# Optimization experiments

Measured on AMD Instinct MI355X. Metric: run time of the kernel, lower is better.

Reference implementation:

```python
import jax, jax.numpy as jnp
import numpy as np

B, K, NUM_CLASS = 16, 256, 18
# strictly-upper-triangle pairs in row-major order, matching torch.nonzero(tril-masked dist < 3)
_iu = np.triu_indices(K, 1)
PAIRS = jnp.stack([jnp.asarray(_iu[0], jnp.int32), jnp.asarray(_iu[1], jnp.int32)], axis=1)  # (P,2)


def _box_intervals(center, size, heading):
    # vectorized getXyz: vectors = diag(diag(size) * R(heading)) = size * [h1, 1, h1]
    h1 = heading[:, 1:2]
    vectors = size * jnp.concatenate([h1, jnp.ones_like(h1), h1], axis=-1)
    low = vectors + center - jnp.abs(size)
    high = vectors + center
    # per-proposal axis-aligned interval [lx,hx,ly,hy,lz,hz]
    return jnp.stack([low[:, 0], high[:, 0], low[:, 1], high[:, 1], low[:, 2], high[:, 2]], axis=-1)  # (K,6)


def _suppress(center, size, heading, scores):
    # center/size (K,3), heading (K,2), scores (K,2); sequential pairwise suppression
    d = _box_intervals(center, size, heading)

    def step(scores, pij):
        i, j = pij[0], pij[1]
        active = jnp.sum((center[i] - center[j]) ** 2) < 9.0  # ||ci-cj|| < 3
        d1, d2 = d[i], d[j]
        case0 = (d2[0] < d1[0]) & (d2[1] > d1[1]) & (d2[2] < d1[2]) & (d2[3] > d1[3]) & (d2[4] < d1[4]) & (d2[5] > d1[5])
        case1 = (d2[0] > d1[0]) & (d2[1] < d1[1]) & (d2[2] > d1[2]) & (d2[3] < d1[3]) & (d2[4] > d1[4]) & (d2[5] < d1[5])

        def ov(lo1, hi1, lo2, hi2):
            return ((hi2 > lo1) & (hi2 < hi1)) | ((hi1 > lo2) & (hi1 < hi2))

        case2 = ov(d1[0], d1[1], d2[0], d2[1]) & ov(d1[2], d1[3], d2[2], d2[3]) & ov(d1[4], d1[5], d2[4], d2[5])
        zp, zn = scores[i, 0], scores[i, 1]
        fp, fn = scores[j, 0], scores[j, 1]
        c2 = (~case0) & (~case1) & case2
        swap_i = active & ((case0 & (zp < zn)) | (c2 & (zn < fn)))
        swap_j = active & ((((~case0) & case1) & (fp < fn)) | (c2 & ~(zn < fn)))
        scores = scores.at[i].set(jnp.where(swap_i, jnp.stack([zn, zp]), jnp.stack([zp, zn])))
        scores = scores.at[j].set(jnp.where(swap_j, jnp.stack([fn, fp]), jnp.stack([fp, fn])))
        return scores, None

    scores, _ = jax.lax.scan(step, scores, PAIRS)
    return scores


def _forward(pred_center, pred_size, pred_heading, sem_obj_feature, aggregated_vote_xyz):
    # decode_scores
    center = aggregated_vote_xyz + jnp.transpose(pred_center, (0, 2, 1))  # (B,K,3)
    size = jnp.transpose(pred_size, (0, 2, 1))                           # (B,K,3)
    heading = jnp.transpose(pred_heading, (0, 2, 1))                     # (B,K,2)
    sem_obj = jnp.transpose(sem_obj_feature, (0, 2, 1))                  # (B,K,2+NUM_CLASS)
    obj = jax.vmap(_suppress)(center, size, heading, sem_obj[..., 0:2])  # post_process
    sem_cls = sem_obj[..., 2:]
    return jnp.concatenate([center, size, heading, obj, sem_cls], axis=-1)  # (B,K,28)


def setup_inputs() -> dict:
    key = jax.random.key(0)
    k1, k2, k3, k4, k5 = jax.random.split(key, 5)
    return {
        "pred_center": jax.random.normal(k1, (B, 3, K), jnp.float32) * 0.2,
        "pred_size": jax.random.uniform(k2, (B, 3, K), jnp.float32, minval=0.1, maxval=2.0),
        "pred_heading": jax.random.normal(k3, (B, 2, K), jnp.float32),
        "sem_obj_feature": jax.random.normal(k4, (B, 2 + NUM_CLASS, K), jnp.float32),
        "aggregated_vote_xyz": jax.random.normal(k5, (B, K, 3), jnp.float32) * 3.0,
    }


def reference(pred_center, pred_size, pred_heading, sem_obj_feature, aggregated_vote_xyz):
    return _forward(pred_center, pred_size, pred_heading, sem_obj_feature, aggregated_vote_xyz)
```

## Files before the change

kernel.cpp:

```cpp
#include <hip/hip_runtime.h>

#define KK 256
#define NCLS 18
#define MASK_BYTES_PER_BATCH (KK * KK)

typedef unsigned long long ull;

__global__ __launch_bounds__(256)
void flags_kernel(const float* __restrict__ pc, const float* __restrict__ ps,
                  const float* __restrict__ ph, const float* __restrict__ sem,
                  const float* __restrict__ av,
                  unsigned char* __restrict__ ws_mask,
                  unsigned char* __restrict__ ws_sum,
                  float* __restrict__ out)
{
#pragma clang fp contract(off)
    const int blk = blockIdx.x;
    const int b   = blk >> 4;
    const int g   = blk & 15;
    const int tid = threadIdx.x;

    __shared__ float sd0[KK], sd1[KK], sd2[KK], sd3[KK], sd4[KK], sd5[KK];
    __shared__ float sp[KK], sn[KK], sc0[KK], sc1[KK], sc2[KK];
    __shared__ unsigned rowsum[16];

    const float* pcb  = pc  + (size_t)b * 3 * KK;
    const float* psb  = ps  + (size_t)b * 3 * KK;
    const float* phb  = ph  + (size_t)b * 2 * KK;
    const float* semb = sem + (size_t)b * (2 + NCLS) * KK;
    const float* avb  = av  + (size_t)b * KK * 3;
    float* outb       = out + (size_t)b * KK * 28;

    {
        const int k = tid;
        const float c0 = avb[k*3+0] + pcb[0*KK + k];
        const float c1 = avb[k*3+1] + pcb[1*KK + k];
        const float c2 = avb[k*3+2] + pcb[2*KK + k];
        const float s0 = psb[0*KK + k], s1 = psb[1*KK + k], s2 = psb[2*KK + k];
        const float h1 = phb[1*KK + k];
        const float v0 = s0 * h1, v1 = s1, v2 = s2 * h1;
        sd0[k] = (v0 + c0) - fabsf(s0);
        sd1[k] = (v0 + c0);
        sd2[k] = (v1 + c1) - fabsf(s1);
        sd3[k] = (v1 + c1);
        sd4[k] = (v2 + c2) - fabsf(s2);
        sd5[k] = (v2 + c2);
        sp[k]  = semb[0*KK + k];
        sn[k]  = semb[1*KK + k];
        sc0[k] = c0; sc1[k] = c1; sc2[k] = c2;
    }
    if (tid < 16) rowsum[tid] = 0;
    __syncthreads();

    const int rl = tid & 15;
    const int i  = g * 16 + rl;
    const int j0 = (tid >> 4) * 16;

    const float piv = sp[i], niv = sn[i];
    const float di0 = sd0[i], di1 = sd1[i], di2 = sd2[i];
    const float di3 = sd3[i], di4 = sd4[i], di5 = sd5[i];
    const float ci0 = sc0[i], ci1 = sc1[i], ci2 = sc2[i];

    unsigned W[4] = {0u, 0u, 0u, 0u};
    bool evt = false;
#pragma unroll
    for (int t = 0; t < 16; ++t) {
        const int j = j0 + t;
        unsigned a0 = 1u, a1 = 1u, b0 = 0u, b1 = 0u, isC = 0u, mm0 = 0u, mm1 = 1u;
        if (j > i) {
            const float dx = ci0 - sc0[j];
            const float dy = ci1 - sc1[j];
            const float dz = ci2 - sc2[j];
            const float dist2 = dx*dx + dy*dy + dz*dz;
            if (dist2 < 9.0f) {
                const float e0 = sd0[j], e1 = sd1[j], e2 = sd2[j];
                const float e3 = sd3[j], e4 = sd4[j], e5 = sd5[j];
                const bool case0 = (e0 < di0) & (e1 > di1) & (e2 < di2)
                                 & (e3 > di3) & (e4 < di4) & (e5 > di5);
                const bool case1 = (e0 > di0) & (e1 < di1) & (e2 > di2)
                                 & (e3 < di3) & (e4 > di4) & (e5 < di5);
                if (case0) {
                    const unsigned tA0 = (piv < niv) ? 1u : 0u;
                    const unsigned tA1 = (niv < piv) ? 0u : 1u;
                    a0 = a1 = tA0 ^ tA1;
                    b0 = b1 = tA0;
                    evt = true;
                } else if (case1) {
                    const float pjv = sp[j], njv = sn[j];
                    mm0 = (pjv < njv) ? 1u : 0u;
                    mm1 = (njv < pjv) ? 0u : 1u;
                    evt = true;
                } else {
                    const bool ovx = ((e1 > di0) & (e1 < di1)) | ((di1 > e0) & (di1 < e1));
                    const bool ovy = ((e3 > di2) & (e3 < di3)) | ((di3 > e2) & (di3 < e3));
                    const bool ovz = ((e5 > di4) & (e5 < di5)) | ((di5 > e4) & (di5 < e5));
                    if (ovx & ovy & ovz) {
                        const float pjv = sp[j], njv = sn[j];
                        const unsigned c00 = (niv < njv) ? 1u : 0u;
                        const unsigned c10 = (piv < njv) ? 1u : 0u;
                        const unsigned c01 = (niv < pjv) ? 1u : 0u;
                        const unsigned c11 = (piv < pjv) ? 1u : 0u;
                        isC = 1u;
                        a0 = 1u ^ c00 ^ c10;  b0 = c00;
                        a1 = 1u ^ c01 ^ c11;  b1 = c01;
                        evt = true;
                    }
                }
            }
        }
        const unsigned s = a0 | (a1 << 4) | (b0 << 8) | (b1 << 12)
                         | (isC << 16) | (mm0 << 20) | (mm1 << 24);
        W[t >> 2] |= s << (t & 3);
    }

    uint4 w4;
    w4.x = W[0]; w4.y = W[1]; w4.z = W[2]; w4.w = W[3];
    *(uint4*)(ws_mask + (size_t)b * MASK_BYTES_PER_BATCH + i * KK + j0) = w4;

    if (evt) atomicOr(&rowsum[rl], 1u);

    for (int s = tid; s < 16 * 28; s += 256) {
        const int kk = g * 16 + (s / 28);
        const int c  = s % 28;
        if (c == 8 || c == 9) continue;
        float val;
        if (c < 3)       val = (c == 0) ? sc0[kk] : ((c == 1) ? sc1[kk] : sc2[kk]);
        else if (c < 6)  val = psb[(c - 3) * KK + kk];
        else if (c < 8)  val = phb[(c - 6) * KK + kk];
        else             val = semb[(c - 8) * KK + kk];
        outb[(size_t)kk * 28 + c] = val;
    }

    __syncthreads();
    if (tid < 16) {
        ws_sum[b * KK + g * 16 + tid] = (unsigned char)rowsum[tid];
    }
}

__global__ __launch_bounds__(64)
void suppress7_kernel(const float* __restrict__ sem,
                      const unsigned char* __restrict__ ws_mask,
                      const unsigned char* __restrict__ ws_sum,
                      float* __restrict__ out)
{
    const int b    = blockIdx.x;
    const int lane = threadIdx.x;

    __shared__ unsigned s_mask[KK * 64];

    const float* semb = sem + (size_t)b * (2 + NCLS) * KK;
    float* outb       = out + (size_t)b * KK * 28;

    const uint4* gm = (const uint4*)(ws_mask + (size_t)b * MASK_BYTES_PER_BATCH);
    uint4* sm4 = (uint4*)s_mask;
    for (int so = 0; so < 64; so += 8) {
        uint4 v[8];
#pragma unroll
        for (int t = 0; t < 8; ++t) v[t] = gm[(so + t) * 64 + lane];
#pragma unroll
        for (int t = 0; t < 8; ++t) sm4[(so + t) * 64 + lane] = v[t];
    }

    float pj[4], nj[4];
#pragma unroll
    for (int q = 0; q < 4; ++q) {
        const int k = lane * 4 + q;
        pj[q] = semb[0*KK + k];
        nj[q] = semb[1*KK + k];
    }

    const unsigned char* sbp = ws_sum + b * KK;
    const unsigned sb0 = sbp[lane], sb1 = sbp[64 + lane],
                   sb2 = sbp[128 + lane], sb3 = sbp[192 + lane];
    const ull any0 = __ballot(sb0 & 1u);
    const ull any1 = __ballot(sb1 & 1u);
    const ull any2 = __ballot(sb2 & 1u);
    const ull any3 = __ballot(sb3 & 1u);

    __syncthreads();

    unsigned bmask = 0;
    const ull belowR = __builtin_bitreverse64((1ull << lane) - 1ull);

#define ROWBODY(i_) { \
        const unsigned m = mcur; \
        const int slot = (i_) & 3, owner = (i_) >> 2; \
        const ull bsb = __ballot(((bmask >> slot) & 1u) != 0u); \
        const unsigned b_start = (unsigned)((bsb >> owner) & 1ull); \
        const unsigned A0n = m & 0xFu,         A1n = (m >> 4) & 0xFu; \
        const unsigned B0n = (m >> 8) & 0xFu,  B1n = (m >> 12) & 0xFu; \
        const unsigned isCn = (m >> 16) & 0xFu; \
        const unsigned M0n = (m >> 20) & 0xFu, M1n = (m >> 24) & 0xFu; \
        const unsigned bm = bmask; \
        const unsigned AV  = (A1n & bm) | (A0n & ~bm); \
        const unsigned BV  = (B1n & bm) | (B0n & ~bm); \
        const unsigned bmB = (M1n & bm) | (M0n & ~bm); \
        const unsigned F0s = isCn & ~BV; \
        const unsigned F1s = isCn & (AV ^ BV); \
         \
        const unsigned As = AV << 1; \
        const unsigned Bs = BV << 1; \
        const unsigned B2 = Bs ^ (As & (Bs << 1)); \
        const unsigned A2 = As & (As << 1); \
        const unsigned av0 = B2 ^ (A2 & (B2 << 2)); \
        const unsigned y  = As | 1u; \
        const unsigned z1 = y & ((y << 1) | 1u); \
        const unsigned pa = z1 & ((z1 << 2) | 3u); \
        const unsigned FS  = (AV & av0) ^ BV;    \
        const unsigned aTv = pa & AV;            \
        const ull b0m = __ballot((FS & 8u) != 0u); \
        const ull b1m = __ballot(((FS ^ aTv) & 8u) != 0u); \
         \
        const ull nm  = b0m & ~b1m; \
        const ull cm  = ~(b0m ^ b1m); \
        const ull cmr = __builtin_bitreverse64(cm); \
        const ull nmr = __builtin_bitreverse64(nm); \
        const ull Wr  = __builtin_bitreverse64(b0m); \
        const ull cbr = cmr & belowR; \
        const ull lb  = cbr & (0ull - cbr); \
        const unsigned vK = ((Wr & lb) != 0ull) ? 1u : 0u; \
        const ull betw = belowR & (lb - 1ull); \
        const unsigned par = (unsigned)__builtin_popcountll(nmr & betw) & 1u; \
        const unsigned excl = ((cbr != 0ull) ? vK : b_start) ^ par; \
        const ull lbA = cmr & (0ull - cmr); \
        const unsigned vKA = ((Wr & lbA) != 0ull) ? 1u : 0u; \
        const unsigned parA = (unsigned)__builtin_popcountll(nmr & (lbA - 1ull)) & 1u; \
        const unsigned bfin = ((cmr != 0ull) ? vKA : b_start) ^ parA; \
         \
        const unsigned Emask = (0u - excl) & 0xFu; \
        const unsigned sv = av0 ^ (pa & Emask); \
        const unsigned flips = (F1s & sv) | (F0s & ~sv); \
        unsigned nbm = bmB ^ flips; \
        const unsigned fixed = (nbm & ~(1u << slot)) | (bfin << slot); \
        bmask = (lane == owner) ? fixed : nbm; }

#define RUNCHUNK(W_, ANY, NROWS) \
    for (int bb = 0; bb < (NROWS); ++bb) { \
        const int i_ = ((W_) << 6) + bb; \
        const unsigned mnext = s_mask[(i_ + 1) * 64 + lane]; \
        if (((ANY) >> bb) & 1ull) ROWBODY(i_) \
        mcur = mnext; \
    }

    unsigned mcur = s_mask[lane];
    RUNCHUNK(0, any0, 64)
    RUNCHUNK(1, any1, 64)
    RUNCHUNK(2, any2, 64)
    RUNCHUNK(3, any3, 63)

#undef RUNCHUNK
#undef ROWBODY

#pragma unroll
    for (int q = 0; q < 4; ++q) {
        const int k = lane * 4 + q;
        const unsigned bq = (bmask >> q) & 1u;
        outb[k*28 + 8] = bq ? nj[q] : pj[q];
        outb[k*28 + 9] = bq ? pj[q] : nj[q];
    }
}

__device__ __forceinline__ unsigned compose2(unsigned a, unsigned b) {
    unsigned r0 = (b >> (a & 1u)) & 1u;
    unsigned r1 = (b >> ((a >> 1) & 1u)) & 1u;
    return r0 | (r1 << 1u);
}

__global__ __launch_bounds__(64)
void proposal_suppress_kernel(const float* __restrict__ pc, const float* __restrict__ ps,
                              const float* __restrict__ ph, const float* __restrict__ sem,
                              const float* __restrict__ av, float* __restrict__ out)
{
#pragma clang fp contract(off)
    const int b    = blockIdx.x;
    const int lane = threadIdx.x;

    __shared__ float s_p[KK], s_n[KK], s_d[KK][6], s_c[KK][3];

    const float* pcb  = pc  + (size_t)b * 3 * KK;
    const float* psb  = ps  + (size_t)b * 3 * KK;
    const float* phb  = ph  + (size_t)b * 2 * KK;
    const float* semb = sem + (size_t)b * (2 + NCLS) * KK;
    const float* avb  = av  + (size_t)b * KK * 3;
    float* outb       = out + (size_t)b * KK * 28;

    float pj[4], nj[4], dj[4][6], cj[4][3];
    unsigned Ljm = 0, Gjm = 0, bmask = 0;

#pragma unroll
    for (int q = 0; q < 4; ++q) {
        const int k = lane * 4 + q;
        const float c0 = avb[k*3+0] + pcb[0*KK + k];
        const float c1 = avb[k*3+1] + pcb[1*KK + k];
        const float c2 = avb[k*3+2] + pcb[2*KK + k];
        const float s0 = psb[0*KK + k], s1 = psb[1*KK + k], s2 = psb[2*KK + k];
        const float h0 = phb[0*KK + k], h1 = phb[1*KK + k];
        const float v0 = s0 * h1, v1 = s1, v2 = s2 * h1;
        float d[6];
        d[0] = (v0 + c0) - fabsf(s0); d[1] = (v0 + c0);
        d[2] = (v1 + c1) - fabsf(s1); d[3] = (v1 + c1);
        d[4] = (v2 + c2) - fabsf(s2); d[5] = (v2 + c2);
        const float p = semb[0*KK + k];
        const float n = semb[1*KK + k];
        cj[q][0] = c0; cj[q][1] = c1; cj[q][2] = c2;
#pragma unroll
        for (int m = 0; m < 6; ++m) dj[q][m] = d[m];
        pj[q] = p; nj[q] = n;
        if (p < n) Ljm |= 1u << q;
        if (n < p) Gjm |= 1u << q;
        s_p[k] = p; s_n[k] = n;
#pragma unroll
        for (int m = 0; m < 6; ++m) s_d[k][m] = d[m];
        s_c[k][0] = c0; s_c[k][1] = c1; s_c[k][2] = c2;
        outb[k*28 + 0] = c0; outb[k*28 + 1] = c1; outb[k*28 + 2] = c2;
        outb[k*28 + 3] = s0; outb[k*28 + 4] = s1; outb[k*28 + 5] = s2;
        outb[k*28 + 6] = h0; outb[k*28 + 7] = h1;
#pragma unroll
        for (int cc = 0; cc < NCLS; ++cc)
            outb[k*28 + 10 + cc] = semb[(2 + cc)*KK + k];
    }
    __syncthreads();

    const unsigned ID = 2u;
    for (int i = 0; i < KK - 1; ++i) {
        const float piv = s_p[i], niv = s_n[i];
        const float di0 = s_d[i][0], di1 = s_d[i][1], di2 = s_d[i][2];
        const float di3 = s_d[i][3], di4 = s_d[i][4], di5 = s_d[i][5];
        const float ci0 = s_c[i][0], ci1 = s_c[i][1], ci2 = s_c[i][2];
        const unsigned tA = (piv < niv ? 1u : 0u) | ((niv < piv ? 0u : 1u) << 1);
        const int owner = i >> 2, slot = i & 3;

        unsigned tq[4];
        unsigned Cq = 0, cc0m = 0, cc1m = 0;
        unsigned tl = ID;
#pragma unroll
        for (int q = 0; q < 4; ++q) {
            const int j = lane * 4 + q;
            unsigned t = ID;
            if (j > i) {
                const float dx = ci0 - cj[q][0];
                const float dy = ci1 - cj[q][1];
                const float dz = ci2 - cj[q][2];
                const float dist2 = dx*dx + dy*dy + dz*dz;
                if (dist2 < 9.0f) {
                    const bool case0 = (dj[q][0] < di0) & (dj[q][1] > di1)
                                     & (dj[q][2] < di2) & (dj[q][3] > di3)
                                     & (dj[q][4] < di4) & (dj[q][5] > di5);
                    const bool case1 = (dj[q][0] > di0) & (dj[q][1] < di1)
                                     & (dj[q][2] > di2) & (dj[q][3] < di3)
                                     & (dj[q][4] > di4) & (dj[q][5] < di5);
                    if (case0) {
                        t = tA;
                    } else if (case1) {
                        const unsigned bj = (bmask >> q) & 1u;
                        const unsigned nb = bj ? (((Gjm >> q) & 1u) ? 0u : 1u)
                                               : (((Ljm >> q) & 1u) ? 1u : 0u);
                        bmask = (bmask & ~(1u << q)) | (nb << q);
                    } else {
                        const bool ovx = ((dj[q][1] > di0) & (dj[q][1] < di1))
                                       | ((di1 > dj[q][0]) & (di1 < dj[q][1]));
                        const bool ovy = ((dj[q][3] > di2) & (dj[q][3] < di3))
                                       | ((di3 > dj[q][2]) & (di3 < dj[q][3]));
                        const bool ovz = ((dj[q][5] > di4) & (dj[q][5] < di5))
                                       | ((di5 > dj[q][4]) & (di5 < dj[q][5]));
                        if (ovx & ovy & ovz) {
                            const unsigned bj = (bmask >> q) & 1u;
                            const float sj = bj ? pj[q] : nj[q];
                            const unsigned c0b = (niv < sj) ? 1u : 0u;
                            const unsigned c1b = (piv < sj) ? 1u : 0u;
                            t = c0b | ((c1b ^ 1u) << 1u);
                            Cq |= 1u << q; cc0m |= c0b << q; cc1m |= c1b << q;
                        }
                    }
                }
            }
            tq[q] = t;
            tl = compose2(tl, t);
        }

        const ull any = __ballot((tl != ID) || (Cq != 0));
        if (any == 0ull) continue;

        const unsigned b_start = (((unsigned)__shfl((int)bmask, owner, 64)) >> slot) & 1u;

        unsigned incl = tl;
#pragma unroll
        for (int off = 1; off < 64; off <<= 1) {
            const unsigned other = (unsigned)__shfl_up((int)incl, (unsigned)off, 64);
            if (lane >= off) incl = compose2(other, incl);
        }
        const unsigned total = (unsigned)__shfl((int)incl, 63, 64);
        const unsigned upv   = (unsigned)__shfl_up((int)incl, 1u, 64);
        const unsigned excl  = (lane == 0) ? ID : upv;

        unsigned cur = (excl >> b_start) & 1u;
#pragma unroll
        for (int q = 0; q < 4; ++q) {
            if ((Cq >> q) & 1u) {
                const unsigned cond = cur ? ((cc1m >> q) & 1u) : ((cc0m >> q) & 1u);
                if (!cond) bmask ^= (1u << q);
            }
            cur = (tq[q] >> cur) & 1u;
        }
        if (lane == owner) {
            const unsigned nbi = (total >> b_start) & 1u;
            bmask = (bmask & ~(1u << slot)) | (nbi << slot);
        }
    }

#pragma unroll
    for (int q = 0; q < 4; ++q) {
        const int k = lane * 4 + q;
        const unsigned bq = (bmask >> q) & 1u;
        outb[k*28 + 8] = bq ? nj[q] : pj[q];
        outb[k*28 + 9] = bq ? pj[q] : nj[q];
    }
}

extern "C" void kernel_launch(void* const* d_in, const int* in_sizes, int n_in,
                              void* d_out, int out_size, void* d_ws, size_t ws_size,
                              hipStream_t stream) {
    const float* pc  = (const float*)d_in[0];
    const float* ps  = (const float*)d_in[1];
    const float* ph  = (const float*)d_in[2];
    const float* sem = (const float*)d_in[3];
    const float* av  = (const float*)d_in[4];
    float* out = (float*)d_out;
    const int B = in_sizes[0] / (3 * KK);

    const size_t need = (size_t)B * MASK_BYTES_PER_BATCH + (size_t)B * KK;
    if (ws_size >= need) {
        unsigned char* wm   = (unsigned char*)d_ws;
        unsigned char* wsum = wm + (size_t)B * MASK_BYTES_PER_BATCH;
        flags_kernel<<<dim3(B * 16), dim3(256), 0, stream>>>(pc, ps, ph, sem, av, wm, wsum, out);
        suppress7_kernel<<<dim3(B), dim3(64), 0, stream>>>(sem, wm, wsum, out);
    } else {
        proposal_suppress_kernel<<<dim3(B), dim3(64), 0, stream>>>(pc, ps, ph, sem, av, out);
    }
}
```

Measured before the change: 43.98 us.

## Replace row-skip flags with branchless log-step parallel prefix scan in suppression

Removes the per-row event summary (rowsum atomics, extra sync and ws_sum buffer) from the flags kernel, so the suppression kernel no longer skips rows with no interactions. The cross-lane carry in each row changes from bit-reverse, lowest-set-bit and popcount logic to a six-step log-shift scan over the 64-bit ballot masks. Both outcomes for each lane are computed and one is picked per lane. This shortens the serial dependency chain per row and drops a workspace write and a barrier, but every one of the 255 rows is now processed even when it has no events.

Result: slower. 78.69 us (+78.9%).

```diff
diff --git a/kernel.cpp b/kernel.cpp
--- a/kernel.cpp
+++ b/kernel.cpp
@@ -11,7 +11,6 @@
                   const float* __restrict__ ph, const float* __restrict__ sem,
                   const float* __restrict__ av,
                   unsigned char* __restrict__ ws_mask,
-                  unsigned char* __restrict__ ws_sum,
                   float* __restrict__ out)
 {
 #pragma clang fp contract(off)
@@ -22,7 +21,6 @@
 
     __shared__ float sd0[KK], sd1[KK], sd2[KK], sd3[KK], sd4[KK], sd5[KK];
     __shared__ float sp[KK], sn[KK], sc0[KK], sc1[KK], sc2[KK];
-    __shared__ unsigned rowsum[16];
 
     const float* pcb  = pc  + (size_t)b * 3 * KK;
     const float* psb  = ps  + (size_t)b * 3 * KK;
@@ -49,7 +47,6 @@
         sn[k]  = semb[1*KK + k];
         sc0[k] = c0; sc1[k] = c1; sc2[k] = c2;
     }
-    if (tid < 16) rowsum[tid] = 0;
     __syncthreads();
 
     const int rl = tid & 15;
@@ -62,7 +59,6 @@
     const float ci0 = sc0[i], ci1 = sc1[i], ci2 = sc2[i];
 
     unsigned W[4] = {0u, 0u, 0u, 0u};
-    bool evt = false;
 #pragma unroll
     for (int t = 0; t < 16; ++t) {
         const int j = j0 + t;
@@ -84,12 +80,10 @@
                     const unsigned tA1 = (niv < piv) ? 0u : 1u;
                     a0 = a1 = tA0 ^ tA1;
                     b0 = b1 = tA0;
-                    evt = true;
                 } else if (case1) {
                     const float pjv = sp[j], njv = sn[j];
                     mm0 = (pjv < njv) ? 1u : 0u;
                     mm1 = (njv < pjv) ? 0u : 1u;
-                    evt = true;
                 } else {
                     const bool ovx = ((e1 > di0) & (e1 < di1)) | ((di1 > e0) & (di1 < e1));
                     const bool ovy = ((e3 > di2) & (e3 < di3)) | ((di3 > e2) & (di3 < e3));
@@ -103,7 +97,6 @@
                         isC = 1u;
                         a0 = 1u ^ c00 ^ c10;  b0 = c00;
                         a1 = 1u ^ c01 ^ c11;  b1 = c01;
-                        evt = true;
                     }
                 }
             }
@@ -116,8 +109,6 @@
     uint4 w4;
     w4.x = W[0]; w4.y = W[1]; w4.z = W[2]; w4.w = W[3];
     *(uint4*)(ws_mask + (size_t)b * MASK_BYTES_PER_BATCH + i * KK + j0) = w4;
-
-    if (evt) atomicOr(&rowsum[rl], 1u);
 
     for (int s = tid; s < 16 * 28; s += 256) {
         const int kk = g * 16 + (s / 28);
@@ -130,17 +121,11 @@
         else             val = semb[(c - 8) * KK + kk];
         outb[(size_t)kk * 28 + c] = val;
     }
-
-    __syncthreads();
-    if (tid < 16) {
-        ws_sum[b * KK + g * 16 + tid] = (unsigned char)rowsum[tid];
-    }
 }
 
 __global__ __launch_bounds__(64)
-void suppress7_kernel(const float* __restrict__ sem,
+void suppress8_kernel(const float* __restrict__ sem,
                       const unsigned char* __restrict__ ws_mask,
-                      const unsigned char* __restrict__ ws_sum,
                       float* __restrict__ out)
 {
     const int b    = blockIdx.x;
@@ -169,87 +154,72 @@
         nj[q] = semb[1*KK + k];
     }
 
-    const unsigned char* sbp = ws_sum + b * KK;
-    const unsigned sb0 = sbp[lane], sb1 = sbp[64 + lane],
-                   sb2 = sbp[128 + lane], sb3 = sbp[192 + lane];
-    const ull any0 = __ballot(sb0 & 1u);
-    const ull any1 = __ballot(sb1 & 1u);
-    const ull any2 = __ballot(sb2 & 1u);
-    const ull any3 = __ballot(sb3 & 1u);
-
     __syncthreads();
 
     unsigned bmask = 0;
-    const ull belowR = __builtin_bitreverse64((1ull << lane) - 1ull);
-
-#define ROWBODY(i_) { \
-        const unsigned m = mcur; \
-        const int slot = (i_) & 3, owner = (i_) >> 2; \
-        const ull bsb = __ballot(((bmask >> slot) & 1u) != 0u); \
-        const unsigned b_start = (unsigned)((bsb >> owner) & 1ull); \
-        const unsigned A0n = m & 0xFu,         A1n = (m >> 4) & 0xFu; \
-        const unsigned B0n = (m >> 8) & 0xFu,  B1n = (m >> 12) & 0xFu; \
-        const unsigned isCn = (m >> 16) & 0xFu; \
-        const unsigned M0n = (m >> 20) & 0xFu, M1n = (m >> 24) & 0xFu; \
-        const unsigned bm = bmask; \
-        const unsigned AV  = (A1n & bm) | (A0n & ~bm); \
-        const unsigned BV  = (B1n & bm) | (B0n & ~bm); \
-        const unsigned bmB = (M1n & bm) | (M0n & ~bm); \
-        const unsigned F0s = isCn & ~BV; \
-        const unsigned F1s = isCn & (AV ^ BV); \
-         \
-        const unsigned As = AV << 1; \
-        const unsigned Bs = BV << 1; \
-        const unsigned B2 = Bs ^ (As & (Bs << 1)); \
-        const unsigned A2 = As & (As << 1); \
-        const unsigned av0 = B2 ^ (A2 & (B2 << 2)); \
-        const unsigned y  = As | 1u; \
-        const unsigned z1 = y & ((y << 1) | 1u); \
-        const unsigned pa = z1 & ((z1 << 2) | 3u); \
-        const unsigned FS  = (AV & av0) ^ BV;    \
-        const unsigned aTv = pa & AV;            \
-        const ull b0m = __ballot((FS & 8u) != 0u); \
-        const ull b1m = __ballot(((FS ^ aTv) & 8u) != 0u); \
-         \
-        const ull nm  = b0m & ~b1m; \
-        const ull cm  = ~(b0m ^ b1m); \
-        const ull cmr = __builtin_bitreverse64(cm); \
-        const ull nmr = __builtin_bitreverse64(nm); \
-        const ull Wr  = __builtin_bitreverse64(b0m); \
-        const ull cbr = cmr & belowR; \
-        const ull lb  = cbr & (0ull - cbr); \
-        const unsigned vK = ((Wr & lb) != 0ull) ? 1u : 0u; \
-        const ull betw = belowR & (lb - 1ull); \
-        const unsigned par = (unsigned)__builtin_popcountll(nmr & betw) & 1u; \
-        const unsigned excl = ((cbr != 0ull) ? vK : b_start) ^ par; \
-        const ull lbA = cmr & (0ull - cmr); \
-        const unsigned vKA = ((Wr & lbA) != 0ull) ? 1u : 0u; \
-        const unsigned parA = (unsigned)__builtin_popcountll(nmr & (lbA - 1ull)) & 1u; \
-        const unsigned bfin = ((cmr != 0ull) ? vKA : b_start) ^ parA; \
-         \
-        const unsigned Emask = (0u - excl) & 0xFu; \
-        const unsigned sv = av0 ^ (pa & Emask); \
-        const unsigned flips = (F1s & sv) | (F0s & ~sv); \
-        unsigned nbm = bmB ^ flips; \
-        const unsigned fixed = (nbm & ~(1u << slot)) | (bfin << slot); \
-        bmask = (lane == owner) ? fixed : nbm; }
-
-#define RUNCHUNK(W_, ANY, NROWS) \
-    for (int bb = 0; bb < (NROWS); ++bb) { \
-        const int i_ = ((W_) << 6) + bb; \
-        const unsigned mnext = s_mask[(i_ + 1) * 64 + lane]; \
-        if (((ANY) >> bb) & 1ull) ROWBODY(i_) \
-        mcur = mnext; \
-    }
-
     unsigned mcur = s_mask[lane];
-    RUNCHUNK(0, any0, 64)
-    RUNCHUNK(1, any1, 64)
-    RUNCHUNK(2, any2, 64)
-    RUNCHUNK(3, any3, 63)
-
-#undef RUNCHUNK
-#undef ROWBODY
+
+    for (int i = 0; i < KK - 1; ++i) {
+        const unsigned mnext = s_mask[(i + 1) * 64 + lane];
+        const unsigned m = mcur;
+        const int slot = i & 3, owner = i >> 2;
+
+        const ull bsb = __ballot(((bmask >> slot) & 1u) != 0u);
+
+        const unsigned A0n = m & 0xFu,         A1n = (m >> 4) & 0xFu;
+        const unsigned B0n = (m >> 8) & 0xFu,  B1n = (m >> 12) & 0xFu;
+        const unsigned isCn = (m >> 16) & 0xFu;
+        const unsigned M0n = (m >> 20) & 0xFu, M1n = (m >> 24) & 0xFu;
+        const unsigned bm = bmask;
+        const unsigned AV  = (A1n & bm) | (A0n & ~bm);
+        const unsigned BV  = (B1n & bm) | (B0n & ~bm);
+        const unsigned bmB = (M1n & bm) | (M0n & ~bm);
+        const unsigned F0s = isCn & ~BV;
+        const unsigned F1s = isCn & (AV ^ BV);
+
+        const unsigned As = AV << 1;
+        const unsigned Bs = BV << 1;
+        const unsigned B2 = Bs ^ (As & (Bs << 1));
+        const unsigned A2 = As & (As << 1);
+        const unsigned av0 = B2 ^ (A2 & (B2 << 2));
+        const unsigned y  = As | 1u;
+        const unsigned z1 = y & ((y << 1) | 1u);
+        const unsigned pa = z1 & ((z1 << 2) | 3u);
+        const unsigned FS  = (AV & av0) ^ BV;
+        const unsigned aTv = pa & AV;
+
+        const ull b0m = __ballot((FS & 8u) != 0u);
+        const ull b1m = __ballot(((FS ^ aTv) & 8u) != 0u);
+
+        const unsigned sv1 = av0 ^ pa;
+        const unsigned flips0 = (F1s & av0) | (F0s & ~av0);
+        const unsigned flips1 = (F1s & sv1) | (F0s & ~sv1);
+        const unsigned nbm0 = bmB ^ flips0;
+        const unsigned nbm1 = bmB ^ flips1;
+
+        const ull amask = b0m ^ b1m;
+        ull A = (amask << 1) | 1ull;
+        ull B = b0m << 1;
+        B ^= A & (B << 1);  A &= (A << 1)  | 1ull;
+        B ^= A & (B << 2);  A &= (A << 2)  | 3ull;
+        B ^= A & (B << 4);  A &= (A << 4)  | 15ull;
+        B ^= A & (B << 8);  A &= (A << 8)  | 255ull;
+        B ^= A & (B << 16); A &= (A << 16) | 0xFFFFull;
+        B ^= A & (B << 32); A &= (A << 32) | 0xFFFFFFFFull;
+        const unsigned b_start = (unsigned)((bsb >> owner) & 1ull);
+        const ull EW = B ^ (b_start ? A : 0ull);
+        const unsigned bfin = (unsigned)(((amask & EW) ^ b0m) >> 63) & 1u;
+
+        const unsigned keep = ~(1u << slot);
+        const unsigned ins  = bfin << slot;
+        const unsigned fixed0 = (lane == owner) ? ((nbm0 & keep) | ins) : nbm0;
+        const unsigned fixed1 = (lane == owner) ? ((nbm1 & keep) | ins) : nbm1;
+
+        const unsigned El = (unsigned)((EW >> lane) & 1ull);
+        bmask = El ? fixed1 : fixed0;
+
+        mcur = mnext;
+    }
 
 #pragma unroll
     for (int q = 0; q < 4; ++q) {
@@ -428,12 +398,11 @@
     float* out = (float*)d_out;
     const int B = in_sizes[0] / (3 * KK);
 
-    const size_t need = (size_t)B * MASK_BYTES_PER_BATCH + (size_t)B * KK;
+    const size_t need = (size_t)B * MASK_BYTES_PER_BATCH;
     if (ws_size >= need) {
-        unsigned char* wm   = (unsigned char*)d_ws;
-        unsigned char* wsum = wm + (size_t)B * MASK_BYTES_PER_BATCH;
-        flags_kernel<<<dim3(B * 16), dim3(256), 0, stream>>>(pc, ps, ph, sem, av, wm, wsum, out);
-        suppress7_kernel<<<dim3(B), dim3(64), 0, stream>>>(sem, wm, wsum, out);
+        unsigned char* wm = (unsigned char*)d_ws;
+        flags_kernel<<<dim3(B * 16), dim3(256), 0, stream>>>(pc, ps, ph, sem, av, wm, out);
+        suppress8_kernel<<<dim3(B), dim3(64), 0, stream>>>(sem, wm, out);
     } else {
         proposal_suppress_kernel<<<dim3(B), dim3(64), 0, stream>>>(pc, ps, ph, sem, av, out);
     }
```

## Process two batches per wavefront in suppression kernel to interleave serial chains

Applied to the files above, without the earlier changes.

The sequential suppression kernel now handles two batch elements per 64-lane block, interleaving their per-row dependency chains so the latency of ballots and bit operations in one chain can be hidden by the other. The grid is halved and LDS use doubles to 128KB per block. The cost is fewer blocks (8 instead of 16) and longer per-block work. The gain depends on whether interleaving two serial chains hides latency better than running them on separate CUs.

Result: slower. 64.25 us (+46.1%).

```diff
diff --git a/kernel.cpp b/kernel.cpp
--- a/kernel.cpp
+++ b/kernel.cpp
@@ -138,60 +138,78 @@
 }
 
 __global__ __launch_bounds__(64)
-void suppress7_kernel(const float* __restrict__ sem,
-                      const unsigned char* __restrict__ ws_mask,
-                      const unsigned char* __restrict__ ws_sum,
-                      float* __restrict__ out)
+void suppress11_kernel(const float* __restrict__ sem,
+                       const unsigned char* __restrict__ ws_mask,
+                       const unsigned char* __restrict__ ws_sum,
+                       float* __restrict__ out, int B)
 {
-    const int b    = blockIdx.x;
+    const int pb   = blockIdx.x;
+    const int bA   = pb * 2;
+    const int bBr  = pb * 2 + 1;
+    const bool hasB = (bBr < B);
+    const int bB   = hasB ? bBr : bA;
     const int lane = threadIdx.x;
 
-    __shared__ unsigned s_mask[KK * 64];
-
-    const float* semb = sem + (size_t)b * (2 + NCLS) * KK;
-    float* outb       = out + (size_t)b * KK * 28;
-
-    const uint4* gm = (const uint4*)(ws_mask + (size_t)b * MASK_BYTES_PER_BATCH);
-    uint4* sm4 = (uint4*)s_mask;
+    __shared__ unsigned s_mask[2 * KK * 64];
+
+    const float* sembA = sem + (size_t)bA * (2 + NCLS) * KK;
+    const float* sembB = sem + (size_t)bB * (2 + NCLS) * KK;
+    float* outbA = out + (size_t)bA * KK * 28;
+    float* outbB = out + (size_t)bB * KK * 28;
+
+    const uint4* gmA = (const uint4*)(ws_mask + (size_t)bA * MASK_BYTES_PER_BATCH);
+    const uint4* gmB = (const uint4*)(ws_mask + (size_t)bB * MASK_BYTES_PER_BATCH);
+    uint4* smA = (uint4*)s_mask;
+    uint4* smB = (uint4*)(s_mask + KK * 64);
     for (int so = 0; so < 64; so += 8) {
-        uint4 v[8];
-#pragma unroll
-        for (int t = 0; t < 8; ++t) v[t] = gm[(so + t) * 64 + lane];
-#pragma unroll
-        for (int t = 0; t < 8; ++t) sm4[(so + t) * 64 + lane] = v[t];
-    }
-
-    float pj[4], nj[4];
+        uint4 v[8], w[8];
+#pragma unroll
+        for (int t = 0; t < 8; ++t) v[t] = gmA[(so + t) * 64 + lane];
+#pragma unroll
+        for (int t = 0; t < 8; ++t) w[t] = gmB[(so + t) * 64 + lane];
+#pragma unroll
+        for (int t = 0; t < 8; ++t) smA[(so + t) * 64 + lane] = v[t];
+#pragma unroll
+        for (int t = 0; t < 8; ++t) smB[(so + t) * 64 + lane] = w[t];
+    }
+
+    float pjA[4], njA[4], pjB[4], njB[4];
 #pragma unroll
     for (int q = 0; q < 4; ++q) {
         const int k = lane * 4 + q;
-        pj[q] = semb[0*KK + k];
-        nj[q] = semb[1*KK + k];
-    }
-
-    const unsigned char* sbp = ws_sum + b * KK;
-    const unsigned sb0 = sbp[lane], sb1 = sbp[64 + lane],
-                   sb2 = sbp[128 + lane], sb3 = sbp[192 + lane];
-    const ull any0 = __ballot(sb0 & 1u);
-    const ull any1 = __ballot(sb1 & 1u);
-    const ull any2 = __ballot(sb2 & 1u);
-    const ull any3 = __ballot(sb3 & 1u);
+        pjA[q] = sembA[0*KK + k];
+        njA[q] = sembA[1*KK + k];
+        pjB[q] = sembB[0*KK + k];
+        njB[q] = sembB[1*KK + k];
+    }
+
+    const unsigned char* sbA = ws_sum + bA * KK;
+    const unsigned char* sbB = ws_sum + bB * KK;
+    const unsigned a0 = sbA[lane], a1 = sbA[64 + lane],
+                   a2 = sbA[128 + lane], a3 = sbA[192 + lane];
+    const unsigned e0 = sbB[lane], e1 = sbB[64 + lane],
+                   e2 = sbB[128 + lane], e3 = sbB[192 + lane];
+    const ull anyA0 = __ballot(a0 & 1u), anyA1 = __ballot(a1 & 1u),
+              anyA2 = __ballot(a2 & 1u), anyA3 = __ballot(a3 & 1u);
+    ull anyB0 = __ballot(e0 & 1u), anyB1 = __ballot(e1 & 1u),
+        anyB2 = __ballot(e2 & 1u), anyB3 = __ballot(e3 & 1u);
+    if (!hasB) { anyB0 = anyB1 = anyB2 = anyB3 = 0ull; }
 
     __syncthreads();
 
-    unsigned bmask = 0;
+    unsigned bmaskA = 0, bmaskB = 0;
     const ull belowR = __builtin_bitreverse64((1ull << lane) - 1ull);
 
-#define ROWBODY(i_) { \
-        const unsigned m = mcur; \
+#define ROWBODY(i_, MW, BMV) { \
+        const unsigned m = (MW); \
         const int slot = (i_) & 3, owner = (i_) >> 2; \
-        const ull bsb = __ballot(((bmask >> slot) & 1u) != 0u); \
+        const ull bsb = __ballot(((BMV >> slot) & 1u) != 0u); \
         const unsigned b_start = (unsigned)((bsb >> owner) & 1ull); \
         const unsigned A0n = m & 0xFu,         A1n = (m >> 4) & 0xFu; \
         const unsigned B0n = (m >> 8) & 0xFu,  B1n = (m >> 12) & 0xFu; \
         const unsigned isCn = (m >> 16) & 0xFu; \
         const unsigned M0n = (m >> 20) & 0xFu, M1n = (m >> 24) & 0xFu; \
-        const unsigned bm = bmask; \
+        const unsigned bm = BMV; \
         const unsigned AV  = (A1n & bm) | (A0n & ~bm); \
         const unsigned BV  = (B1n & bm) | (B0n & ~bm); \
         const unsigned bmB = (M1n & bm) | (M0n & ~bm); \
@@ -232,21 +250,24 @@
         const unsigned flips = (F1s & sv) | (F0s & ~sv); \
         unsigned nbm = bmB ^ flips; \
         const unsigned fixed = (nbm & ~(1u << slot)) | (bfin << slot); \
-        bmask = (lane == owner) ? fixed : nbm; }
-
-#define RUNCHUNK(W_, ANY, NROWS) \
+        BMV = (lane == owner) ? fixed : nbm; }
+
+#define RUNCHUNK(W_, ANYA, ANYB, NROWS) \
     for (int bb = 0; bb < (NROWS); ++bb) { \
         const int i_ = ((W_) << 6) + bb; \
-        const unsigned mnext = s_mask[(i_ + 1) * 64 + lane]; \
-        if (((ANY) >> bb) & 1ull) ROWBODY(i_) \
-        mcur = mnext; \
-    }
-
-    unsigned mcur = s_mask[lane];
-    RUNCHUNK(0, any0, 64)
-    RUNCHUNK(1, any1, 64)
-    RUNCHUNK(2, any2, 64)
-    RUNCHUNK(3, any3, 63)
+        const unsigned mnextA = s_mask[(i_ + 1) * 64 + lane]; \
+        const unsigned mnextB = s_mask[KK * 64 + (i_ + 1) * 64 + lane]; \
+        if (((ANYA) >> bb) & 1ull) ROWBODY(i_, mcurA, bmaskA) \
+        if (((ANYB) >> bb) & 1ull) ROWBODY(i_, mcurB, bmaskB) \
+        mcurA = mnextA; mcurB = mnextB; \
+    }
+
+    unsigned mcurA = s_mask[lane];
+    unsigned mcurB = s_mask[KK * 64 + lane];
+    RUNCHUNK(0, anyA0, anyB0, 64)
+    RUNCHUNK(1, anyA1, anyB1, 64)
+    RUNCHUNK(2, anyA2, anyB2, 64)
+    RUNCHUNK(3, anyA3, anyB3, 63)
 
 #undef RUNCHUNK
 #undef ROWBODY
@@ -254,9 +275,18 @@
 #pragma unroll
     for (int q = 0; q < 4; ++q) {
         const int k = lane * 4 + q;
-        const unsigned bq = (bmask >> q) & 1u;
-        outb[k*28 + 8] = bq ? nj[q] : pj[q];
-        outb[k*28 + 9] = bq ? pj[q] : nj[q];
+        const unsigned bqA = (bmaskA >> q) & 1u;
+        outbA[k*28 + 8] = bqA ? njA[q] : pjA[q];
+        outbA[k*28 + 9] = bqA ? pjA[q] : njA[q];
+    }
+    if (hasB) {
+#pragma unroll
+        for (int q = 0; q < 4; ++q) {
+            const int k = lane * 4 + q;
+            const unsigned bqB = (bmaskB >> q) & 1u;
+            outbB[k*28 + 8] = bqB ? njB[q] : pjB[q];
+            outbB[k*28 + 9] = bqB ? pjB[q] : njB[q];
+        }
     }
 }
 
@@ -433,7 +463,7 @@
         unsigned char* wm   = (unsigned char*)d_ws;
         unsigned char* wsum = wm + (size_t)B * MASK_BYTES_PER_BATCH;
         flags_kernel<<<dim3(B * 16), dim3(256), 0, stream>>>(pc, ps, ph, sem, av, wm, wsum, out);
-        suppress7_kernel<<<dim3(B), dim3(64), 0, stream>>>(sem, wm, wsum, out);
+        suppress11_kernel<<<dim3((B + 1) / 2), dim3(64), 0, stream>>>(sem, wm, wsum, out, B);
     } else {
         proposal_suppress_kernel<<<dim3(B), dim3(64), 0, stream>>>(pc, ps, ph, sem, av, out);
     }
```
